# Optimization experiments

Measured on AMD Instinct MI355X. Metric: run time of the kernel, lower is better.

Reference implementation:

```python
import jax, jax.numpy as jnp
import numpy as np

N = 50000       # nodes
E = 800000      # edges (before self-loops)
F = 128         # input features
H = 4           # heads
C = 64          # hidden per head
NC = 40         # classes
NEG_SLOPE = 0.2  # PyG GATConv default leaky relu slope


def _glorot(key, shape):
    fan = sum(shape[-2:]) if len(shape) >= 2 else shape[-1] * 2
    return jax.random.normal(key, shape, jnp.float32) * jnp.sqrt(2.0 / fan)


def gat_conv(x, W, a_src, a_dst, bias, src, dst, concat):
    """PyG-style GATConv (eval mode, self-loops already in src/dst).
    x:[N,Fin] W:[Fin,H*C] a_src,a_dst:[H,C] bias:[H*C] or [C]."""
    n = x.shape[0]
    h_, c_ = a_src.shape
    h = (x @ W).reshape(n, h_, c_)                      # [N,H,C]
    al_s = jnp.einsum('nhc,hc->nh', h, a_src)           # [N,H]
    al_d = jnp.einsum('nhc,hc->nh', h, a_dst)
    logits = jax.nn.leaky_relu(al_s[src] + al_d[dst], NEG_SLOPE)  # [E,H]
    # segment softmax over incoming edges of each dst node
    mx = jax.ops.segment_max(logits, dst, num_segments=n)
    mx = jnp.where(jnp.isfinite(mx), mx, 0.0)
    ex = jnp.exp(logits - mx[dst])
    den = jax.ops.segment_sum(ex, dst, num_segments=n)
    alpha = ex / (den[dst] + 1e-16)                     # [E,H]
    msg = h[src] * alpha[:, :, None]                    # [E,H,C]
    out = jax.ops.segment_sum(msg, dst, num_segments=n) # [N,H,C]
    if concat:
        return out.reshape(n, h_ * c_) + bias
    return out.mean(axis=1) + bias


def setup_inputs() -> dict:
    key = jax.random.key(0)
    ks = jax.random.split(key, 16)
    x = jax.random.normal(ks[0], (N, F), jnp.float32)
    edge_index = jax.random.randint(ks[1], (2, E), 0, N, jnp.int64)
    HC = H * C
    return {
        'x': x, 'edge_index': edge_index,
        'W1': _glorot(ks[2], (F, HC)),   'a1_src': _glorot(ks[3], (H, C)),
        'a1_dst': _glorot(ks[4], (H, C)), 'b1': jnp.zeros((HC,), jnp.float32),
        'W2': _glorot(ks[5], (HC, HC)),  'a2_src': _glorot(ks[6], (H, C)),
        'a2_dst': _glorot(ks[7], (H, C)), 'b2': jnp.zeros((HC,), jnp.float32),
        'W3': _glorot(ks[8], (HC, H * NC)), 'a3_src': _glorot(ks[9], (H, NC)),
        'a3_dst': _glorot(ks[10], (H, NC)), 'b3': jnp.zeros((NC,), jnp.float32),
    }


def reference(x, edge_index, W1, a1_src, a1_dst, b1, W2, a2_src, a2_dst, b2,
              W3, a3_src, a3_dst, b3):
    n = x.shape[0]
    loop = jnp.arange(n, dtype=edge_index.dtype)
    src = jnp.concatenate([edge_index[0], loop])
    dst = jnp.concatenate([edge_index[1], loop])
    x1 = jax.nn.elu(gat_conv(x, W1, a1_src, a1_dst, b1, src, dst, True))
    x2 = jax.nn.elu(gat_conv(x1, W2, a2_src, a2_dst, b2, src, dst, True) + x1)
    out = gat_conv(x2, W3, a3_src, a3_dst, b3, src, dst, False)  # [N,NC]
    return out
```

## Files before the change

### kernel.cpp

```cpp
#include <hip/hip_runtime.h>
#include <hip/hip_bf16.h>
#include <hip/hip_fp16.h>
#include <math.h>

#define NEG_SLOPE 0.2f

typedef _Float16 half8 __attribute__((ext_vector_type(8)));
typedef _Float16 half4 __attribute__((ext_vector_type(4)));
typedef float f32x4 __attribute__((ext_vector_type(4)));

__global__ void degree_kernel(const int* __restrict__ ei, int E, int n,
                              int* __restrict__ deg) {
    int e = blockIdx.x * 256 + threadIdx.x;
    int tot = E + n;
    if (e >= tot) return;
    int d = (e < E) ? ei[E + e] : (e - E);
    atomicAdd(&deg[d], 1);
}

__global__ __launch_bounds__(1024) void scan_block(const int* __restrict__ deg,
                                                   int* __restrict__ row_off,
                                                   int* __restrict__ bsums, int n) {
    __shared__ int tmp[1024];
    int t = threadIdx.x;
    int idx = blockIdx.x * 1024 + t;
    int v = (idx < n) ? deg[idx] : 0;
    tmp[t] = v;
    __syncthreads();
    #pragma unroll
    for (int off = 1; off < 1024; off <<= 1) {
        int x = (t >= off) ? tmp[t - off] : 0;
        __syncthreads();
        tmp[t] += x;
        __syncthreads();
    }
    if (idx < n) row_off[idx] = tmp[t] - v;
    if (t == 1023) bsums[blockIdx.x] = tmp[1023];
}

__global__ __launch_bounds__(64) void scan_sums(int* __restrict__ bsums, int nb,
                                                int* __restrict__ row_off, int n) {
    int lane = threadIdx.x;
    int carry = 0;
    for (int base = 0; base < nb; base += 64) {
        int i = base + lane;
        int o = (i < nb) ? bsums[i] : 0;
        int v = o;
        #pragma unroll
        for (int off = 1; off < 64; off <<= 1) {
            int x = __shfl_up(v, off, 64);
            if (lane >= off) v += x;
        }
        if (i < nb) bsums[i] = carry + v - o;
        int tot = __shfl(v, 63, 64);
        carry += tot;
    }
    if (lane == 0) row_off[n] = carry;
}

__global__ __launch_bounds__(1024) void scan_add(int* __restrict__ row_off,
                                                 const int* __restrict__ bsums,
                                                 int* __restrict__ cursor, int n) {
    int idx = blockIdx.x * 1024 + threadIdx.x;
    if (idx < n) {
        int v = row_off[idx] + bsums[blockIdx.x];
        row_off[idx] = v;
        cursor[idx] = v;
    }
}

__global__ void scatter_kernel(const int* __restrict__ ei, int E, int n,
                               int* __restrict__ cursor, int* __restrict__ csr_src) {
    int e = blockIdx.x * 256 + threadIdx.x;
    int tot = E + n;
    if (e >= tot) return;
    int s, d;
    if (e < E) { s = ei[e]; d = ei[E + e]; } else { s = d = e - E; }
    int pos = atomicAdd(&cursor[d], 1);
    csr_src[pos] = s;
}

__global__ void split_f32x4(const float* __restrict__ src, _Float16* __restrict__ hi,
                            _Float16* __restrict__ lo, int n4) {
    int i = blockIdx.x * 256 + threadIdx.x;
    if (i >= n4) return;
    float4 v = ((const float4*)src)[i];
    half4 h, l;
    h.x = (_Float16)v.x; l.x = (_Float16)(v.x - (float)h.x);
    h.y = (_Float16)v.y; l.y = (_Float16)(v.y - (float)h.y);
    h.z = (_Float16)v.z; l.z = (_Float16)(v.z - (float)h.z);
    h.w = (_Float16)v.w; l.w = (_Float16)(v.w - (float)h.w);
    ((half4*)hi)[i] = h;
    ((half4*)lo)[i] = l;
}

__global__ void wt_split(const float* __restrict__ W, _Float16* __restrict__ bhi,
                         _Float16* __restrict__ blo, int K, int N, int padN) {
    int idx = blockIdx.x * 256 + threadIdx.x;
    if (idx >= padN * K) return;
    int n = idx / K, k = idx % K;
    float v = (n < N) ? W[(size_t)k * N + n] : 0.f;
    _Float16 h = (_Float16)v;
    bhi[idx] = h;
    blo[idx] = (_Float16)(v - (float)h);
}

__global__ __launch_bounds__(256) void gemm_mfma(const _Float16* __restrict__ Ahi,
                                                 const _Float16* __restrict__ Alo,
                                                 const _Float16* __restrict__ Bthi,
                                                 const _Float16* __restrict__ Btlo,
                                                 _Float16* __restrict__ Ch,
                                                 const float* __restrict__ a_src,
                                                 const float* __restrict__ a_dst,
                                                 float* __restrict__ als,
                                                 float* __restrict__ ald,
                                                 int M, int N, int K) {
    __shared__ _Float16 Ah[2][2][128 * 32];
    int t = threadIdx.x;
    int wave = t >> 6, lane = t & 63;
    int row0 = blockIdx.x * 128, col0 = blockIdx.y * 128;
    int wr = wave >> 1, wc = wave & 1;

    f32x4 acc[4][4];
    #pragma unroll
    for (int i = 0; i < 4; i++)
        #pragma unroll
        for (int j = 0; j < 4; j++)
            acc[i][j] = (f32x4)0.f;

    auto lds_off = [](int m, int g0) -> int {
        int P = m >> 1;
        int gp = ((m & 1) << 2) | g0;
        return P * 64 + ((gp ^ (P & 7)) << 3);
    };

    int s0 = t, s1 = t + 256;
    int r0 = s0 >> 2, g00 = s0 & 3;
    int r1 = s1 >> 2, g01 = s1 & 3;
    int off0 = lds_off(r0, g00), off1 = lds_off(r1, g01);
    bool m0ok = (row0 + r0) < M, m1ok = (row0 + r1) < M;
    const _Float16* a0h = Ahi + (size_t)(row0 + r0) * K + g00 * 8;
    const _Float16* a0l = Alo + (size_t)(row0 + r0) * K + g00 * 8;
    const _Float16* a1h = Ahi + (size_t)(row0 + r1) * K + g01 * 8;
    const _Float16* a1l = Alo + (size_t)(row0 + r1) * K + g01 * 8;

    half8 svh0, svl0, svh1, svl1;
    auto stage_load = [&](int k0) {
        svh0 = svl0 = svh1 = svl1 = (half8)(_Float16)0.f;
        if (m0ok) { svh0 = *(const half8*)(a0h + k0); svl0 = *(const half8*)(a0l + k0); }
        if (m1ok) { svh1 = *(const half8*)(a1h + k0); svl1 = *(const half8*)(a1l + k0); }
    };
    auto stage_write = [&](int buf) {
        *(half8*)(&Ah[buf][0][off0]) = svh0;
        *(half8*)(&Ah[buf][1][off0]) = svl0;
        *(half8*)(&Ah[buf][0][off1]) = svh1;
        *(half8*)(&Ah[buf][1][off1]) = svl1;
    };

    int nk = K >> 5;
    stage_load(0);
    stage_write(0);
    __syncthreads();

    const _Float16* bhp[4];
    const _Float16* blp[4];
    #pragma unroll
    for (int nf = 0; nf < 4; nf++) {
        int n = col0 + wc * 64 + nf * 16 + (lane & 15);
        bhp[nf] = Bthi + (size_t)n * K + (lane >> 4) * 8;
        blp[nf] = Btlo + (size_t)n * K + (lane >> 4) * 8;
    }

    for (int kt = 0; kt < nk; kt++) {
        int cur = kt & 1;
        if (kt + 1 < nk) stage_load((kt + 1) << 5);

        int k0 = kt << 5;
        half8 bh[4], bl[4];
        #pragma unroll
        for (int nf = 0; nf < 4; nf++) {
            bh[nf] = *(const half8*)(bhp[nf] + k0);
            bl[nf] = *(const half8*)(blp[nf] + k0);
        }
        half8 ah[4], al[4];
        #pragma unroll
        for (int mf = 0; mf < 4; mf++) {
            int m = wr * 64 + mf * 16 + (lane & 15);
            int off = lds_off(m, lane >> 4);
            ah[mf] = *(half8*)(&Ah[cur][0][off]);
            al[mf] = *(half8*)(&Ah[cur][1][off]);
        }
        #pragma unroll
        for (int mf = 0; mf < 4; mf++)
            #pragma unroll
            for (int nf = 0; nf < 4; nf++) {
                acc[mf][nf] = __builtin_amdgcn_mfma_f32_16x16x32_f16(
                    ah[mf], bh[nf], acc[mf][nf], 0, 0, 0);
                acc[mf][nf] = __builtin_amdgcn_mfma_f32_16x16x32_f16(
                    ah[mf], bl[nf], acc[mf][nf], 0, 0, 0);
                acc[mf][nf] = __builtin_amdgcn_mfma_f32_16x16x32_f16(
                    al[mf], bh[nf], acc[mf][nf], 0, 0, 0);
            }
        if (kt + 1 < nk) {
            stage_write(cur ^ 1);
            __syncthreads();
        }
    }

    #pragma unroll
    for (int mf = 0; mf < 4; mf++)
        #pragma unroll
        for (int nf = 0; nf < 4; nf++) {
            int col = col0 + wc * 64 + nf * 16 + (lane & 15);
            if (col >= N) continue;
            #pragma unroll
            for (int q = 0; q < 4; q++) {
                int row = row0 + wr * 64 + mf * 16 + (lane >> 4) * 4 + q;
                if (row < M)
                    Ch[(size_t)row * N + col] = (_Float16)acc[mf][nf][q];
            }
        }

    if (a_src) {
        int hblk = blockIdx.y * 2 + wc;
        float asv[4], adv[4];
        #pragma unroll
        for (int nf = 0; nf < 4; nf++) {
            int cih = nf * 16 + (lane & 15);
            asv[nf] = a_src[hblk * 64 + cih];
            adv[nf] = a_dst[hblk * 64 + cih];
        }
        #pragma unroll
        for (int mf = 0; mf < 4; mf++)
            #pragma unroll
            for (int q = 0; q < 4; q++) {
                float ss = 0.f, sd = 0.f;
                #pragma unroll
                for (int nf = 0; nf < 4; nf++) {
                    float v = acc[mf][nf][q];
                    ss = fmaf(v, asv[nf], ss);
                    sd = fmaf(v, adv[nf], sd);
                }
                #pragma unroll
                for (int off = 8; off >= 1; off >>= 1) {
                    ss += __shfl_xor(ss, off, 64);
                    sd += __shfl_xor(sd, off, 64);
                }
                int row = row0 + wr * 64 + mf * 16 + (lane >> 4) * 4 + q;
                if ((lane & 15) == 0 && row < M) {
                    als[row * 4 + hblk] = ss;
                    ald[row * 4 + hblk] = sd;
                }
            }
    }
}

template <int C>
__global__ __launch_bounds__(256) void coef_kernel(const _Float16* __restrict__ h,
                                                   const float* __restrict__ a_src,
                                                   const float* __restrict__ a_dst,
                                                   float* __restrict__ als,
                                                   float* __restrict__ ald, int n) {
    int wave = threadIdx.x >> 6;
    int lane = threadIdx.x & 63;
    int node = blockIdx.x * 4 + wave;
    if (node >= n) return;
    const _Float16* hr = h + (size_t)node * (4 * C);
    float ps[4], pd[4];
    #pragma unroll
    for (int hh = 0; hh < 4; hh++) {
        float hv = (lane < C) ? (float)hr[hh * C + lane] : 0.f;
        float as_ = (lane < C) ? a_src[hh * C + lane] : 0.f;
        float ad_ = (lane < C) ? a_dst[hh * C + lane] : 0.f;
        ps[hh] = hv * as_;
        pd[hh] = hv * ad_;
    }
    #pragma unroll
    for (int off = 32; off >= 1; off >>= 1) {
        #pragma unroll
        for (int hh = 0; hh < 4; hh++) {
            ps[hh] += __shfl_xor(ps[hh], off, 64);
            pd[hh] += __shfl_xor(pd[hh], off, 64);
        }
    }
    if (lane == 0) {
        #pragma unroll
        for (int hh = 0; hh < 4; hh++) {
            als[node * 4 + hh] = ps[hh];
            ald[node * 4 + hh] = pd[hh];
        }
    }
}

template <int C, int MODE>
__global__ __launch_bounds__(256) void agg_kernel(const __half* __restrict__ hhp,
                                                  const float* __restrict__ als,
                                                  const float* __restrict__ ald,
                                                  const int* __restrict__ row_off,
                                                  const int* __restrict__ csr_src,
                                                  const float* __restrict__ bias,
                                                  const _Float16* __restrict__ rh,
                                                  const _Float16* __restrict__ rl,
                                                  float* __restrict__ outf,
                                                  _Float16* __restrict__ oh,
                                                  _Float16* __restrict__ ol, int n) {
    constexpr int HC = 4 * C;
    constexpr int LPN = HC / 8;
    constexpr int LPH = C / 8;
    const _Float16* hh = (const _Float16*)hhp;

    int t = threadIdx.x;
    int wave = t >> 6, lane = t & 63;
    int l = lane & 31;
    int pairs = (n + 1) >> 1;

    for (int p = blockIdx.x * 4 + wave; p < pairs; p += gridDim.x * 4) {
        int node = p * 2 + (lane >> 5);
        bool nact = node < n;
        bool lact = nact && (l < LPN);
        int g = (l < LPN) ? (l / LPH) : 0;

        int rs = 0, cnt = 0;
        if (lact) {
            rs = row_off[node];
            cnt = row_off[node + 1] - rs;
        }
        float aldg = lact ? ald[node * 4 + g] : 0.f;

        float acc[8] = {};
        float den = 0.f;

        if (cnt > 0) {
            int sA[8];
            float avA[8];
            #pragma unroll
            for (int q = 0; q < 8; q++) {
                int idx = q < cnt ? q : cnt - 1;
                sA[q] = csr_src[rs + idx];
            }
            #pragma unroll
            for (int q = 0; q < 8; q++) avA[q] = als[sA[q] * 4 + g];

            for (int base = 0; base < cnt; base += 8) {
                half8 hv[8];
                #pragma unroll
                for (int q = 0; q < 8; q++)
                    hv[q] = *(const half8*)(hh + (size_t)sA[q] * HC + l * 8);

                int sB[8];
                float avB[8];
                if (base + 8 < cnt) {
                    #pragma unroll
                    for (int q = 0; q < 8; q++) {
                        int idx = base + 8 + q; if (idx >= cnt) idx = cnt - 1;
                        sB[q] = csr_src[rs + idx];
                    }
                    #pragma unroll
                    for (int q = 0; q < 8; q++) avB[q] = als[sB[q] * 4 + g];
                }

                float ex[8];
                #pragma unroll
                for (int q = 0; q < 8; q++) {
                    float lg = avA[q] + aldg;
                    lg = (lg > 0.f) ? lg : NEG_SLOPE * lg;
                    float e = __expf(lg);
                    ex[q] = (base + q < cnt) ? e : 0.f;
                    den += ex[q];
                }
                #pragma unroll
                for (int q = 0; q < 8; q++) {
                    #pragma unroll
                    for (int k = 0; k < 8; k++)
                        acc[k] = fmaf(ex[q], (float)hv[q][k], acc[k]);
                }
                #pragma unroll
                for (int q = 0; q < 8; q++) { sA[q] = sB[q]; avA[q] = avB[q]; }
            }
        }

        float inv = 1.f / (den + 1e-16f);
        float v[8];
        #pragma unroll
        for (int k = 0; k < 8; k++) v[k] = acc[k] * inv;

        if (MODE == 2) {
            float vs[8];
            #pragma unroll
            for (int k = 0; k < 8; k++) vs[k] = v[k];
            #pragma unroll
            for (int k2 = 1; k2 < 4; k2++) {
                #pragma unroll
                for (int k = 0; k < 8; k++)
                    vs[k] += __shfl(v[k], lane + 5 * k2, 64);
            }
            if (nact && l < 5) {
                float b[8];
                *(float4*)&b[0] = *(const float4*)(bias + l * 8);
                *(float4*)&b[4] = *(const float4*)(bias + l * 8 + 4);
                float o[8];
                #pragma unroll
                for (int k = 0; k < 8; k++) o[k] = vs[k] * 0.25f + b[k];
                *(float4*)(outf + (size_t)node * C + l * 8)     = make_float4(o[0], o[1], o[2], o[3]);
                *(float4*)(outf + (size_t)node * C + l * 8 + 4) = make_float4(o[4], o[5], o[6], o[7]);
            }
        } else {
            if (lact) {
                float b[8];
                *(float4*)&b[0] = *(const float4*)(bias + l * 8);
                *(float4*)&b[4] = *(const float4*)(bias + l * 8 + 4);
                float o[8];
                #pragma unroll
                for (int k = 0; k < 8; k++) o[k] = v[k] + b[k];
                if (MODE == 1) {
                    size_t ridx = (size_t)node * HC + l * 8;
                    half8 r_h = *(const half8*)(rh + ridx);
                    half8 r_l = *(const half8*)(rl + ridx);
                    #pragma unroll
                    for (int k = 0; k < 8; k++) o[k] += (float)r_h[k] + (float)r_l[k];
                }
                #pragma unroll
                for (int k = 0; k < 8; k++) o[k] = (o[k] > 0.f) ? o[k] : expm1f(o[k]);
                half8 hv8, lv8;
                #pragma unroll
                for (int k = 0; k < 8; k++) {
                    hv8[k] = (_Float16)o[k];
                    lv8[k] = (_Float16)(o[k] - (float)hv8[k]);
                }
                size_t oidx = (size_t)node * HC + l * 8;
                *(half8*)(oh + oidx) = hv8;
                *(half8*)(ol + oidx) = lv8;
            }
        }
    }
}

extern "C" void kernel_launch(void* const* d_in, const int* in_sizes, int n_in,
                              void* d_out, int out_size, void* d_ws, size_t ws_size,
                              hipStream_t stream) {
    const float* x   = (const float*)d_in[0];
    const int*   ei  = (const int*)d_in[1];
    const float* W1  = (const float*)d_in[2];
    const float* a1s = (const float*)d_in[3];
    const float* a1d = (const float*)d_in[4];
    const float* b1  = (const float*)d_in[5];
    const float* W2  = (const float*)d_in[6];
    const float* a2s = (const float*)d_in[7];
    const float* a2d = (const float*)d_in[8];
    const float* b2  = (const float*)d_in[9];
    const float* W3  = (const float*)d_in[10];
    const float* a3s = (const float*)d_in[11];
    const float* a3d = (const float*)d_in[12];
    const float* b3  = (const float*)d_in[13];
    float* out = (float*)d_out;

    int N = in_sizes[0] / 128;
    int E = in_sizes[1] / 2;

    char* ws = (char*)d_ws;
    size_t off = 0;
    auto alloc = [&](size_t bytes) -> void* {
        void* p = ws + off;
        off += (bytes + 255) & ~(size_t)255;
        return p;
    };
    _Float16* hhalf = (_Float16*)alloc((size_t)N * 256 * 2);
    _Float16* pA_hi = (_Float16*)alloc((size_t)N * 256 * 2);
    _Float16* pA_lo = (_Float16*)alloc((size_t)N * 256 * 2);
    _Float16* pB_hi = (_Float16*)alloc((size_t)N * 256 * 2);
    _Float16* pB_lo = (_Float16*)alloc((size_t)N * 256 * 2);
    float*    als   = (float*)alloc((size_t)N * 4 * 4);
    float*    ald   = (float*)alloc((size_t)N * 4 * 4);
    _Float16* bt1h  = (_Float16*)alloc(256 * 128 * 2);
    _Float16* bt1l  = (_Float16*)alloc(256 * 128 * 2);
    _Float16* bt2h  = (_Float16*)alloc(256 * 256 * 2);
    _Float16* bt2l  = (_Float16*)alloc(256 * 256 * 2);
    _Float16* bt3h  = (_Float16*)alloc(256 * 256 * 2);
    _Float16* bt3l  = (_Float16*)alloc(256 * 256 * 2);
    int* deg     = (int*)alloc((size_t)N * 4);
    int* row_off = (int*)alloc((size_t)(N + 1) * 4);
    int* cursor  = (int*)alloc((size_t)N * 4);
    int* csr     = (int*)alloc((size_t)(E + N) * 4);
    int* bsums   = (int*)alloc(1024 * 4);

    int tot = E + N;
    int nb = (N + 1023) / 1024;
    hipMemsetAsync(deg, 0, (size_t)N * 4, stream);
    degree_kernel<<<(tot + 255) / 256, 256, 0, stream>>>(ei, E, N, deg);
    scan_block<<<nb, 1024, 0, stream>>>(deg, row_off, bsums, N);
    scan_sums<<<1, 64, 0, stream>>>(bsums, nb, row_off, N);
    scan_add<<<nb, 1024, 0, stream>>>(row_off, bsums, cursor, N);
    scatter_kernel<<<(tot + 255) / 256, 256, 0, stream>>>(ei, E, N, cursor, csr);

    {
        int n4 = N * 128 / 4;
        split_f32x4<<<(n4 + 255) / 256, 256, 0, stream>>>(x, pA_hi, pA_lo, n4);
        wt_split<<<(256 * 128 + 255) / 256, 256, 0, stream>>>(W1, bt1h, bt1l, 128, 256, 256);
        wt_split<<<(256 * 256 + 255) / 256, 256, 0, stream>>>(W2, bt2h, bt2l, 256, 256, 256);
        wt_split<<<(256 * 256 + 255) / 256, 256, 0, stream>>>(W3, bt3h, bt3l, 256, 160, 256);
    }

    int nodeBlocks4 = (N + 3) / 4;
    int pairs = (N + 1) / 2;
    int aggBlocks = (pairs + 3) / 4;
    if (aggBlocks > 2048) aggBlocks = 2048;
    dim3 blk(256);
    dim3 ggrid((N + 127) / 128, 2);

    gemm_mfma<<<ggrid, blk, 0, stream>>>(pA_hi, pA_lo, bt1h, bt1l, hhalf,
                                         a1s, a1d, als, ald, N, 256, 128);
    agg_kernel<64, 0><<<aggBlocks, blk, 0, stream>>>((const __half*)hhalf, als, ald,
        row_off, csr, b1, nullptr, nullptr, nullptr, pB_hi, pB_lo, N);

    gemm_mfma<<<ggrid, blk, 0, stream>>>(pB_hi, pB_lo, bt2h, bt2l, hhalf,
                                         a2s, a2d, als, ald, N, 256, 256);
    agg_kernel<64, 1><<<aggBlocks, blk, 0, stream>>>((const __half*)hhalf, als, ald,
        row_off, csr, b2, pB_hi, pB_lo, nullptr, pA_hi, pA_lo, N);

    gemm_mfma<<<ggrid, blk, 0, stream>>>(pA_hi, pA_lo, bt3h, bt3l, hhalf,
                                         nullptr, nullptr, nullptr, nullptr, N, 160, 256);
    coef_kernel<40><<<nodeBlocks4, blk, 0, stream>>>(hhalf, a3s, a3d, als, ald, N);
    agg_kernel<40, 2><<<aggBlocks, blk, 0, stream>>>((const __half*)hhalf, als, ald,
        row_off, csr, b3, nullptr, nullptr, out, nullptr, nullptr, N);
}
```

Before: 488.7 us.

## Retile GEMM to 64-row full-width blocks, prefetch B, merge weight splits, drop agg grid-stride

The GEMM now gives each 64-row block all 256 output columns, with one column-head per wave. K is a compile-time template parameter, the k-loop is fully unrolled, and the next B fragments are prefetched into registers alongside the A staging. This avoids reloading each A row tile for a second column block and hides B global-load latency, at the cost of more blocks and higher register pressure under launch_bounds(256,1). The three weight-split launches are merged into one kernel. The aggregation kernel drops its grid-stride loop and its 2048-block cap, so each wave handles exactly one node pair.

```diff
diff --git a/kernel.cpp b/kernel.cpp
--- a/kernel.cpp
+++ b/kernel.cpp
@@ -94,39 +94,43 @@
     ((half4*)lo)[i] = l;
 }
 
-__global__ void wt_split(const float* __restrict__ W, _Float16* __restrict__ bhi,
-                         _Float16* __restrict__ blo, int K, int N, int padN) {
+__global__ void wt_split_all(const float* __restrict__ W1, const float* __restrict__ W2,
+                             const float* __restrict__ W3,
+                             _Float16* __restrict__ b1h, _Float16* __restrict__ b1l,
+                             _Float16* __restrict__ b2h, _Float16* __restrict__ b2l,
+                             _Float16* __restrict__ b3h, _Float16* __restrict__ b3l) {
     int idx = blockIdx.x * 256 + threadIdx.x;
-    if (idx >= padN * K) return;
-    int n = idx / K, k = idx % K;
+    const float* W; _Float16 *bh, *bl; int K, N, li;
+    if (idx < 256 * 128) {
+        W = W1; bh = b1h; bl = b1l; K = 128; N = 256; li = idx;
+    } else if (idx < 256 * 128 + 256 * 256) {
+        W = W2; bh = b2h; bl = b2l; K = 256; N = 256; li = idx - 256 * 128;
+    } else if (idx < 256 * 128 + 2 * 256 * 256) {
+        W = W3; bh = b3h; bl = b3l; K = 256; N = 160; li = idx - 256 * 128 - 256 * 256;
+    } else return;
+    int n = li / K, k = li % K;
     float v = (n < N) ? W[(size_t)k * N + n] : 0.f;
     _Float16 h = (_Float16)v;
-    bhi[idx] = h;
-    blo[idx] = (_Float16)(v - (float)h);
-}
-
-__global__ __launch_bounds__(256) void gemm_mfma(const _Float16* __restrict__ Ahi,
-                                                 const _Float16* __restrict__ Alo,
-                                                 const _Float16* __restrict__ Bthi,
-                                                 const _Float16* __restrict__ Btlo,
-                                                 _Float16* __restrict__ Ch,
-                                                 const float* __restrict__ a_src,
-                                                 const float* __restrict__ a_dst,
-                                                 float* __restrict__ als,
-                                                 float* __restrict__ ald,
-                                                 int M, int N, int K) {
-    __shared__ _Float16 Ah[2][2][128 * 32];
+    bh[li] = h;
+    bl[li] = (_Float16)(v - (float)h);
+}
+
+template <int NK, bool FUSE>
+__global__ __launch_bounds__(256, 1) void gemm_mfma(const _Float16* __restrict__ Ahi,
+                                                    const _Float16* __restrict__ Alo,
+                                                    const _Float16* __restrict__ Bthi,
+                                                    const _Float16* __restrict__ Btlo,
+                                                    _Float16* __restrict__ Ch,
+                                                    const float* __restrict__ a_src,
+                                                    const float* __restrict__ a_dst,
+                                                    float* __restrict__ als,
+                                                    float* __restrict__ ald,
+                                                    int M, int N) {
+    constexpr int K = NK * 32;
+    __shared__ _Float16 Ah[2][2][64 * 32];
     int t = threadIdx.x;
     int wave = t >> 6, lane = t & 63;
-    int row0 = blockIdx.x * 128, col0 = blockIdx.y * 128;
-    int wr = wave >> 1, wc = wave & 1;
-
-    f32x4 acc[4][4];
-    #pragma unroll
-    for (int i = 0; i < 4; i++)
-        #pragma unroll
-        for (int j = 0; j < 4; j++)
-            acc[i][j] = (f32x4)0.f;
+    int row0 = blockIdx.x * 64;
 
     auto lds_off = [](int m, int g0) -> int {
         int P = m >> 1;
@@ -134,58 +138,64 @@
         return P * 64 + ((gp ^ (P & 7)) << 3);
     };
 
-    int s0 = t, s1 = t + 256;
-    int r0 = s0 >> 2, g00 = s0 & 3;
-    int r1 = s1 >> 2, g01 = s1 & 3;
-    int off0 = lds_off(r0, g00), off1 = lds_off(r1, g01);
-    bool m0ok = (row0 + r0) < M, m1ok = (row0 + r1) < M;
-    const _Float16* a0h = Ahi + (size_t)(row0 + r0) * K + g00 * 8;
-    const _Float16* a0l = Alo + (size_t)(row0 + r0) * K + g00 * 8;
-    const _Float16* a1h = Ahi + (size_t)(row0 + r1) * K + g01 * 8;
-    const _Float16* a1l = Alo + (size_t)(row0 + r1) * K + g01 * 8;
-
-    half8 svh0, svl0, svh1, svl1;
+    int r0 = t >> 2, g0 = t & 3;
+    int off0 = lds_off(r0, g0);
+    bool mok = (row0 + r0) < M;
+    const _Float16* aph = Ahi + (size_t)(row0 + r0) * K + g0 * 8;
+    const _Float16* apl = Alo + (size_t)(row0 + r0) * K + g0 * 8;
+
+    half8 svh, svl;
     auto stage_load = [&](int k0) {
-        svh0 = svl0 = svh1 = svl1 = (half8)(_Float16)0.f;
-        if (m0ok) { svh0 = *(const half8*)(a0h + k0); svl0 = *(const half8*)(a0l + k0); }
-        if (m1ok) { svh1 = *(const half8*)(a1h + k0); svl1 = *(const half8*)(a1l + k0); }
+        svh = svl = (half8)(_Float16)0.f;
+        if (mok) { svh = *(const half8*)(aph + k0); svl = *(const half8*)(apl + k0); }
     };
     auto stage_write = [&](int buf) {
-        *(half8*)(&Ah[buf][0][off0]) = svh0;
-        *(half8*)(&Ah[buf][1][off0]) = svl0;
-        *(half8*)(&Ah[buf][0][off1]) = svh1;
-        *(half8*)(&Ah[buf][1][off1]) = svl1;
+        *(half8*)(&Ah[buf][0][off0]) = svh;
+        *(half8*)(&Ah[buf][1][off0]) = svl;
     };
 
-    int nk = K >> 5;
+    const _Float16* bhp[4];
+    const _Float16* blp[4];
+    #pragma unroll
+    for (int nf = 0; nf < 4; nf++) {
+        int n = wave * 64 + nf * 16 + (lane & 15);
+        bhp[nf] = Bthi + (size_t)n * K + (lane >> 4) * 8;
+        blp[nf] = Btlo + (size_t)n * K + (lane >> 4) * 8;
+    }
+
+    f32x4 acc[4][4];
+    #pragma unroll
+    for (int i = 0; i < 4; i++)
+        #pragma unroll
+        for (int j = 0; j < 4; j++)
+            acc[i][j] = (f32x4)0.f;
+
     stage_load(0);
     stage_write(0);
+    half8 bh[4], bl[4];
+    #pragma unroll
+    for (int nf = 0; nf < 4; nf++) {
+        bh[nf] = *(const half8*)(bhp[nf]);
+        bl[nf] = *(const half8*)(blp[nf]);
+    }
     __syncthreads();
 
-    const _Float16* bhp[4];
-    const _Float16* blp[4];
-    #pragma unroll
-    for (int nf = 0; nf < 4; nf++) {
-        int n = col0 + wc * 64 + nf * 16 + (lane & 15);
-        bhp[nf] = Bthi + (size_t)n * K + (lane >> 4) * 8;
-        blp[nf] = Btlo + (size_t)n * K + (lane >> 4) * 8;
-    }
-
-    for (int kt = 0; kt < nk; kt++) {
+    #pragma unroll
+    for (int kt = 0; kt < NK; kt++) {
         int cur = kt & 1;
-        if (kt + 1 < nk) stage_load((kt + 1) << 5);
-
-        int k0 = kt << 5;
-        half8 bh[4], bl[4];
-        #pragma unroll
-        for (int nf = 0; nf < 4; nf++) {
-            bh[nf] = *(const half8*)(bhp[nf] + k0);
-            bl[nf] = *(const half8*)(blp[nf] + k0);
+        half8 bh2[4], bl2[4];
+        if (kt + 1 < NK) {
+            stage_load((kt + 1) * 32);
+            #pragma unroll
+            for (int nf = 0; nf < 4; nf++) {
+                bh2[nf] = *(const half8*)(bhp[nf] + (kt + 1) * 32);
+                bl2[nf] = *(const half8*)(blp[nf] + (kt + 1) * 32);
+            }
         }
         half8 ah[4], al[4];
         #pragma unroll
         for (int mf = 0; mf < 4; mf++) {
-            int m = wr * 64 + mf * 16 + (lane & 15);
+            int m = mf * 16 + (lane & 15);
             int off = lds_off(m, lane >> 4);
             ah[mf] = *(half8*)(&Ah[cur][0][off]);
             al[mf] = *(half8*)(&Ah[cur][1][off]);
@@ -201,9 +211,11 @@
                 acc[mf][nf] = __builtin_amdgcn_mfma_f32_16x16x32_f16(
                     al[mf], bh[nf], acc[mf][nf], 0, 0, 0);
             }
-        if (kt + 1 < nk) {
+        if (kt + 1 < NK) {
             stage_write(cur ^ 1);
             __syncthreads();
+            #pragma unroll
+            for (int nf = 0; nf < 4; nf++) { bh[nf] = bh2[nf]; bl[nf] = bl2[nf]; }
         }
     }
 
@@ -211,24 +223,23 @@
     for (int mf = 0; mf < 4; mf++)
         #pragma unroll
         for (int nf = 0; nf < 4; nf++) {
-            int col = col0 + wc * 64 + nf * 16 + (lane & 15);
+            int col = wave * 64 + nf * 16 + (lane & 15);
             if (col >= N) continue;
             #pragma unroll
             for (int q = 0; q < 4; q++) {
-                int row = row0 + wr * 64 + mf * 16 + (lane >> 4) * 4 + q;
+                int row = row0 + mf * 16 + (lane >> 4) * 4 + q;
                 if (row < M)
                     Ch[(size_t)row * N + col] = (_Float16)acc[mf][nf][q];
             }
         }
 
-    if (a_src) {
-        int hblk = blockIdx.y * 2 + wc;
+    if (FUSE) {
         float asv[4], adv[4];
         #pragma unroll
         for (int nf = 0; nf < 4; nf++) {
             int cih = nf * 16 + (lane & 15);
-            asv[nf] = a_src[hblk * 64 + cih];
-            adv[nf] = a_dst[hblk * 64 + cih];
+            asv[nf] = a_src[wave * 64 + cih];
+            adv[nf] = a_dst[wave * 64 + cih];
         }
         #pragma unroll
         for (int mf = 0; mf < 4; mf++)
@@ -246,10 +257,10 @@
                     ss += __shfl_xor(ss, off, 64);
                     sd += __shfl_xor(sd, off, 64);
                 }
-                int row = row0 + wr * 64 + mf * 16 + (lane >> 4) * 4 + q;
+                int row = row0 + mf * 16 + (lane >> 4) * 4 + q;
                 if ((lane & 15) == 0 && row < M) {
-                    als[row * 4 + hblk] = ss;
-                    ald[row * 4 + hblk] = sd;
+                    als[row * 4 + wave] = ss;
+                    ald[row * 4 + wave] = sd;
                 }
             }
     }
@@ -312,125 +323,121 @@
     int t = threadIdx.x;
     int wave = t >> 6, lane = t & 63;
     int l = lane & 31;
-    int pairs = (n + 1) >> 1;
-
-    for (int p = blockIdx.x * 4 + wave; p < pairs; p += gridDim.x * 4) {
-        int node = p * 2 + (lane >> 5);
-        bool nact = node < n;
-        bool lact = nact && (l < LPN);
-        int g = (l < LPN) ? (l / LPH) : 0;
-
-        int rs = 0, cnt = 0;
-        if (lact) {
-            rs = row_off[node];
-            cnt = row_off[node + 1] - rs;
-        }
-        float aldg = lact ? ald[node * 4 + g] : 0.f;
-
-        float acc[8] = {};
-        float den = 0.f;
-
-        if (cnt > 0) {
-            int sA[8];
-            float avA[8];
-            #pragma unroll
-            for (int q = 0; q < 8; q++) {
-                int idx = q < cnt ? q : cnt - 1;
-                sA[q] = csr_src[rs + idx];
-            }
-            #pragma unroll
-            for (int q = 0; q < 8; q++) avA[q] = als[sA[q] * 4 + g];
-
-            for (int base = 0; base < cnt; base += 8) {
-                half8 hv[8];
-                #pragma unroll
-                for (int q = 0; q < 8; q++)
-                    hv[q] = *(const half8*)(hh + (size_t)sA[q] * HC + l * 8);
-
-                int sB[8];
-                float avB[8];
-                if (base + 8 < cnt) {
-                    #pragma unroll
-                    for (int q = 0; q < 8; q++) {
-                        int idx = base + 8 + q; if (idx >= cnt) idx = cnt - 1;
-                        sB[q] = csr_src[rs + idx];
-                    }
-                    #pragma unroll
-                    for (int q = 0; q < 8; q++) avB[q] = als[sB[q] * 4 + g];
-                }
-
-                float ex[8];
+    int node = (blockIdx.x * 4 + wave) * 2 + (lane >> 5);
+    bool nact = node < n;
+    bool lact = nact && (l < LPN);
+    int g = (l < LPN) ? (l / LPH) : 0;
+
+    int rs = 0, cnt = 0;
+    if (lact) {
+        rs = row_off[node];
+        cnt = row_off[node + 1] - rs;
+    }
+    float aldg = lact ? ald[node * 4 + g] : 0.f;
+
+    float acc[8] = {};
+    float den = 0.f;
+
+    if (cnt > 0) {
+        int sA[8];
+        float avA[8];
+        #pragma unroll
+        for (int q = 0; q < 8; q++) {
+            int idx = q < cnt ? q : cnt - 1;
+            sA[q] = csr_src[rs + idx];
+        }
+        #pragma unroll
+        for (int q = 0; q < 8; q++) avA[q] = als[sA[q] * 4 + g];
+
+        for (int base = 0; base < cnt; base += 8) {
+            half8 hv[8];
+            #pragma unroll
+            for (int q = 0; q < 8; q++)
+                hv[q] = *(const half8*)(hh + (size_t)sA[q] * HC + l * 8);
+
+            int sB[8];
+            float avB[8];
+            if (base + 8 < cnt) {
                 #pragma unroll
                 for (int q = 0; q < 8; q++) {
-                    float lg = avA[q] + aldg;
-                    lg = (lg > 0.f) ? lg : NEG_SLOPE * lg;
-                    float e = __expf(lg);
-                    ex[q] = (base + q < cnt) ? e : 0.f;
-                    den += ex[q];
+                    int idx = base + 8 + q; if (idx >= cnt) idx = cnt - 1;
+                    sB[q] = csr_src[rs + idx];
                 }
                 #pragma unroll
-                for (int q = 0; q < 8; q++) {
-                    #pragma unroll
-                    for (int k = 0; k < 8; k++)
-                        acc[k] = fmaf(ex[q], (float)hv[q][k], acc[k]);
-                }
-                #pragma unroll
-                for (int q = 0; q < 8; q++) { sA[q] = sB[q]; avA[q] = avB[q]; }
-            }
-        }
-
-        float inv = 1.f / (den + 1e-16f);
-        float v[8];
-        #pragma unroll
-        for (int k = 0; k < 8; k++) v[k] = acc[k] * inv;
-
-        if (MODE == 2) {
-            float vs[8];
-            #pragma unroll
-            for (int k = 0; k < 8; k++) vs[k] = v[k];
-            #pragma unroll
-            for (int k2 = 1; k2 < 4; k2++) {
+                for (int q = 0; q < 8; q++) avB[q] = als[sB[q] * 4 + g];
+            }
+
+            float ex[8];
+            #pragma unroll
+            for (int q = 0; q < 8; q++) {
+                float lg = avA[q] + aldg;
+                lg = (lg > 0.f) ? lg : NEG_SLOPE * lg;
+                float e = __expf(lg);
+                ex[q] = (base + q < cnt) ? e : 0.f;
+                den += ex[q];
+            }
+            #pragma unroll
+            for (int q = 0; q < 8; q++) {
                 #pragma unroll
                 for (int k = 0; k < 8; k++)
-                    vs[k] += __shfl(v[k], lane + 5 * k2, 64);
-            }
-            if (nact && l < 5) {
-                float b[8];
-                *(float4*)&b[0] = *(const float4*)(bias + l * 8);
-                *(float4*)&b[4] = *(const float4*)(bias + l * 8 + 4);
-                float o[8];
+                    acc[k] = fmaf(ex[q], (float)hv[q][k], acc[k]);
+            }
+            #pragma unroll
+            for (int q = 0; q < 8; q++) { sA[q] = sB[q]; avA[q] = avB[q]; }
+        }
+    }
+
+    float inv = 1.f / (den + 1e-16f);
+    float v[8];
+    #pragma unroll
+    for (int k = 0; k < 8; k++) v[k] = acc[k] * inv;
+
+    if (MODE == 2) {
+        float vs[8];
+        #pragma unroll
+        for (int k = 0; k < 8; k++) vs[k] = v[k];
+        #pragma unroll
+        for (int k2 = 1; k2 < 4; k2++) {
+            #pragma unroll
+            for (int k = 0; k < 8; k++)
+                vs[k] += __shfl(v[k], lane + 5 * k2, 64);
+        }
+        if (nact && l < 5) {
+            float b[8];
+            *(float4*)&b[0] = *(const float4*)(bias + l * 8);
+            *(float4*)&b[4] = *(const float4*)(bias + l * 8 + 4);
+            float o[8];
+            #pragma unroll
+            for (int k = 0; k < 8; k++) o[k] = vs[k] * 0.25f + b[k];
+            *(float4*)(outf + (size_t)node * C + l * 8)     = make_float4(o[0], o[1], o[2], o[3]);
+            *(float4*)(outf + (size_t)node * C + l * 8 + 4) = make_float4(o[4], o[5], o[6], o[7]);
+        }
+    } else {
+        if (lact) {
+            float b[8];
+            *(float4*)&b[0] = *(const float4*)(bias + l * 8);
+            *(float4*)&b[4] = *(const float4*)(bias + l * 8 + 4);
+            float o[8];
+            #pragma unroll
+            for (int k = 0; k < 8; k++) o[k] = v[k] + b[k];
+            if (MODE == 1) {
+                size_t ridx = (size_t)node * HC + l * 8;
+                half8 r_h = *(const half8*)(rh + ridx);
+                half8 r_l = *(const half8*)(rl + ridx);
                 #pragma unroll
-                for (int k = 0; k < 8; k++) o[k] = vs[k] * 0.25f + b[k];
-                *(float4*)(outf + (size_t)node * C + l * 8)     = make_float4(o[0], o[1], o[2], o[3]);
-                *(float4*)(outf + (size_t)node * C + l * 8 + 4) = make_float4(o[4], o[5], o[6], o[7]);
-            }
-        } else {
-            if (lact) {
-                float b[8];
-                *(float4*)&b[0] = *(const float4*)(bias + l * 8);
-                *(float4*)&b[4] = *(const float4*)(bias + l * 8 + 4);
-                float o[8];
-                #pragma unroll
-                for (int k = 0; k < 8; k++) o[k] = v[k] + b[k];
-                if (MODE == 1) {
-                    size_t ridx = (size_t)node * HC + l * 8;
-                    half8 r_h = *(const half8*)(rh + ridx);
-                    half8 r_l = *(const half8*)(rl + ridx);
-                    #pragma unroll
-                    for (int k = 0; k < 8; k++) o[k] += (float)r_h[k] + (float)r_l[k];
-                }
-                #pragma unroll
-                for (int k = 0; k < 8; k++) o[k] = (o[k] > 0.f) ? o[k] : expm1f(o[k]);
-                half8 hv8, lv8;
-                #pragma unroll
-                for (int k = 0; k < 8; k++) {
-                    hv8[k] = (_Float16)o[k];
-                    lv8[k] = (_Float16)(o[k] - (float)hv8[k]);
-                }
-                size_t oidx = (size_t)node * HC + l * 8;
-                *(half8*)(oh + oidx) = hv8;
-                *(half8*)(ol + oidx) = lv8;
-            }
+                for (int k = 0; k < 8; k++) o[k] += (float)r_h[k] + (float)r_l[k];
+            }
+            #pragma unroll
+            for (int k = 0; k < 8; k++) o[k] = (o[k] > 0.f) ? o[k] : expm1f(o[k]);
+            half8 hv8, lv8;
+            #pragma unroll
+            for (int k = 0; k < 8; k++) {
+                hv8[k] = (_Float16)o[k];
+                lv8[k] = (_Float16)(o[k] - (float)hv8[k]);
+            }
+            size_t oidx = (size_t)node * HC + l * 8;
+            *(half8*)(oh + oidx) = hv8;
+            *(half8*)(ol + oidx) = lv8;
         }
     }
 }
@@ -495,30 +502,29 @@
     {
         int n4 = N * 128 / 4;
         split_f32x4<<<(n4 + 255) / 256, 256, 0, stream>>>(x, pA_hi, pA_lo, n4);
-        wt_split<<<(256 * 128 + 255) / 256, 256, 0, stream>>>(W1, bt1h, bt1l, 128, 256, 256);
-        wt_split<<<(256 * 256 + 255) / 256, 256, 0, stream>>>(W2, bt2h, bt2l, 256, 256, 256);
-        wt_split<<<(256 * 256 + 255) / 256, 256, 0, stream>>>(W3, bt3h, bt3l, 256, 160, 256);
+        int wtot = 256 * 128 + 2 * 256 * 256;
+        wt_split_all<<<(wtot + 255) / 256, 256, 0, stream>>>(W1, W2, W3,
+            bt1h, bt1l, bt2h, bt2l, bt3h, bt3l);
     }
 
     int nodeBlocks4 = (N + 3) / 4;
     int pairs = (N + 1) / 2;
     int aggBlocks = (pairs + 3) / 4;
-    if (aggBlocks > 2048) aggBlocks = 2048;
     dim3 blk(256);
-    dim3 ggrid((N + 127) / 128, 2);
-
-    gemm_mfma<<<ggrid, blk, 0, stream>>>(pA_hi, pA_lo, bt1h, bt1l, hhalf,
-                                         a1s, a1d, als, ald, N, 256, 128);
+    dim3 ggrid((N + 63) / 64);
+
+    gemm_mfma<4, true><<<ggrid, blk, 0, stream>>>(pA_hi, pA_lo, bt1h, bt1l, hhalf,
+                                                  a1s, a1d, als, ald, N, 256);
     agg_kernel<64, 0><<<aggBlocks, blk, 0, stream>>>((const __half*)hhalf, als, ald,
         row_off, csr, b1, nullptr, nullptr, nullptr, pB_hi, pB_lo, N);
 
-    gemm_mfma<<<ggrid, blk, 0, stream>>>(pB_hi, pB_lo, bt2h, bt2l, hhalf,
-                                         a2s, a2d, als, ald, N, 256, 256);
+    gemm_mfma<8, true><<<ggrid, blk, 0, stream>>>(pB_hi, pB_lo, bt2h, bt2l, hhalf,
+                                                  a2s, a2d, als, ald, N, 256);
     agg_kernel<64, 1><<<aggBlocks, blk, 0, stream>>>((const __half*)hhalf, als, ald,
         row_off, csr, b2, pB_hi, pB_lo, nullptr, pA_hi, pA_lo, N);
 
-    gemm_mfma<<<ggrid, blk, 0, stream>>>(pA_hi, pA_lo, bt3h, bt3l, hhalf,
-                                         nullptr, nullptr, nullptr, nullptr, N, 160, 256);
+    gemm_mfma<8, false><<<ggrid, blk, 0, stream>>>(pA_hi, pA_lo, bt3h, bt3l, hhalf,
+                                                   nullptr, nullptr, nullptr, nullptr, N, 160);
     coef_kernel<40><<<nodeBlocks4, blk, 0, stream>>>(hhalf, a3s, a3d, als, ald, N);
     agg_kernel<40, 2><<<aggBlocks, blk, 0, stream>>>((const __half*)hhalf, als, ald,
         row_off, csr, b3, nullptr, nullptr, out, nullptr, nullptr, N);
```

New measurement: 459.6 us. -5.9%, faster.
